# Kernel optimization log

Measured on AMD Instinct MI355X. Metric: run time of the kernel, lower is better.

The kernel has to match this reference:

```python
import jax, jax.numpy as jnp
import numpy as np

N = 100000      # nodes
E = 1250000     # edges
IN = 128        # in_channels
H = 64          # hidden_channels
L = 2           # num_layers (GCNConv count)
EPS = 1e-5      # BatchNorm eps


def setup_inputs() -> dict:
    key = jax.random.key(0)
    ks = jax.random.split(key, 10)
    x = jax.random.normal(ks[0], (N, IN), jnp.float32)
    edge_index = jax.random.randint(ks[1], (2, E), 0, N, dtype=jnp.int32)
    fc_w = jax.random.normal(ks[2], (IN, H), jnp.float32) / np.sqrt(IN)
    fc_b = jax.random.normal(ks[3], (H,), jnp.float32) * 0.01
    conv_w = jax.random.normal(ks[4], (L, H, H), jnp.float32) / np.sqrt(H)
    conv_b = jax.random.normal(ks[5], (L, H), jnp.float32) * 0.01
    bn_gamma = jnp.ones((L + 1, H), jnp.float32)
    bn_beta = jnp.zeros((L + 1, H), jnp.float32)
    bn_mean = jax.random.normal(ks[6], (L + 1, H), jnp.float32) * 0.1
    bn_var = jax.random.uniform(ks[7], (L + 1, H), jnp.float32) + 0.5
    return {"x": x, "edge_index": edge_index, "fc_w": fc_w, "fc_b": fc_b,
            "conv_w": conv_w, "conv_b": conv_b, "bn_gamma": bn_gamma,
            "bn_beta": bn_beta, "bn_mean": bn_mean, "bn_var": bn_var}


def reference(x, edge_index, fc_w, fc_b, conv_w, conv_b, bn_gamma, bn_beta, bn_mean, bn_var):
    n = x.shape[0]
    loops = jnp.arange(n, dtype=edge_index.dtype)
    src = jnp.concatenate([edge_index[0], loops])   # add self-loops (GCNConv default)
    dst = jnp.concatenate([edge_index[1], loops])
    # symmetric normalization: deg computed on destination, norm = d_s^-1/2 * d_d^-1/2
    deg = jax.ops.segment_sum(jnp.ones_like(dst, x.dtype), dst, num_segments=n)
    dis = jax.lax.rsqrt(deg)                        # deg >= 1 thanks to self-loops
    norm = dis[src] * dis[dst]                      # [E+N]

    def bn(h, i):  # eval-mode BatchNorm1d with running stats
        return (h - bn_mean[i]) * (bn_gamma[i] * jax.lax.rsqrt(bn_var[i] + EPS)) + bn_beta[i]

    h = jax.nn.relu(bn(x @ fc_w + fc_b, 0))         # [N, H]; dropout is identity in eval
    last = h
    for i in range(conv_w.shape[0]):
        hw = h @ conv_w[i]                          # GCNConv: transform then aggregate
        agg = jax.ops.segment_sum(hw[src] * norm[:, None], dst, num_segments=n) + conv_b[i]
        h = jax.nn.relu(bn(agg, i + 1)) + last      # residual to post-fc activation
    return h
```

## Files before the change

kernel.cpp:

```cpp
#include <hip/hip_runtime.h>

#define NNODES 100000
#define NEDGES 1250000
#define IN_CH 128
#define HID 64
#define BN_EPS 1e-5f

#define NPAD 100352
#define BIN_N 256
#define BINW 391
#define BIN_CHUNK 2048
#define BIN_BLOCKS 611
#define BIN_CAP_LDS 16
#define BIN_REGION 10000
#define MM_BLOCKS 1563
#define GBLOCKS 3125
#define ELL_C 32
#define OVF_CAP 65536

typedef __attribute__((ext_vector_type(8))) short s16x8;
typedef __attribute__((ext_vector_type(4))) float f32x4;

__device__ __forceinline__ ushort f2bf(float f) {
    union { float f; unsigned int i; } c;
    c.f = f;
    unsigned int lsb = (c.i >> 16) & 1u;
    return (ushort)((c.i + 0x7FFFu + lsb) >> 16);
}
__device__ __forceinline__ float asf(unsigned int i) {
    union { unsigned int i; float f; } c;
    c.i = i;
    return c.f;
}

__device__ __forceinline__ void ell_insert(int d, int soff, int* slot,
                                           int* ell, int* ovf_n, int2* ovf) {
    int s = atomicAdd(&slot[d], 1);
    if (s < ELL_C) ell[(d << 5) + s] = soff;
    else {
        int oi = atomicAdd(ovf_n, 1);
        if (oi < OVF_CAP) ovf[oi] = make_int2(d, soff);
    }
}

__device__ __forceinline__ void fc_body(
        int blk, int tid,
        const float* __restrict__ x, const float* __restrict__ w,
        const float* __restrict__ bb,
        const float* __restrict__ g, const float* __restrict__ be,
        const float* __restrict__ mu, const float* __restrict__ var,
        ushort* __restrict__ h0) {
    const int wave = tid >> 6;
    const int lane = tid & 63;
    const int m = lane & 15;
    const int q = lane >> 4;
    const int node_base = (blk * 4 + wave) * 16;

    s16x8 bfrag[4][4];
#pragma unroll
    for (int kc = 0; kc < 4; ++kc)
#pragma unroll
        for (int ct = 0; ct < 4; ++ct)
#pragma unroll
            for (int j = 0; j < 8; ++j)
                bfrag[kc][ct][j] = (short)f2bf(w[(kc * 32 + q * 8 + j) * HID + ct * 16 + m]);

    f32x4 acc[4] = {{0,0,0,0},{0,0,0,0},{0,0,0,0},{0,0,0,0}};

    int row = node_base + m;
    if (row >= NNODES) row = NNODES - 1;
    const float4* xp = (const float4*)(x + (size_t)row * IN_CH + q * 8);

#pragma unroll
    for (int kc = 0; kc < 4; ++kc) {
        float4 a0 = xp[kc * 8 + 0];
        float4 a1 = xp[kc * 8 + 1];
        s16x8 af;
        af[0] = (short)f2bf(a0.x); af[1] = (short)f2bf(a0.y);
        af[2] = (short)f2bf(a0.z); af[3] = (short)f2bf(a0.w);
        af[4] = (short)f2bf(a1.x); af[5] = (short)f2bf(a1.y);
        af[6] = (short)f2bf(a1.z); af[7] = (short)f2bf(a1.w);
#pragma unroll
        for (int ct = 0; ct < 4; ++ct)
            acc[ct] = __builtin_amdgcn_mfma_f32_16x16x32_bf16(af, bfrag[kc][ct], acc[ct], 0, 0, 0);
    }

#pragma unroll
    for (int ct = 0; ct < 4; ++ct) {
        int col = ct * 16 + m;
        float sc = g[col] * rsqrtf(var[col] + BN_EPS);
        float off = (bb[col] - mu[col]) * sc + be[col];
#pragma unroll
        for (int r = 0; r < 4; ++r) {
            int node = node_base + q * 4 + r;
            if (node < NNODES)
                h0[(size_t)node * HID + col] =
                    f2bf(fmaxf(acc[ct][r] * sc + off, 0.f));
        }
    }
}

__global__ __launch_bounds__(256) void bin_fc(
        const int* __restrict__ src, const int* __restrict__ dst,
        unsigned int* __restrict__ staged, int* bin_n,
        int* slot, int* __restrict__ ell, int* ovf_n, int2* __restrict__ ovf,
        const float* __restrict__ x, const float* __restrict__ w,
        const float* __restrict__ bb,
        const float* __restrict__ g, const float* __restrict__ be,
        const float* __restrict__ mu, const float* __restrict__ var,
        ushort* __restrict__ h0) {
    __shared__ unsigned int sbin[BIN_N][BIN_CAP_LDS];
    __shared__ int scnt[BIN_N];
    __shared__ int sbase[BIN_N];
    const int tid = threadIdx.x;

    if (blockIdx.x >= BIN_BLOCKS) {
        fc_body(blockIdx.x - BIN_BLOCKS, tid, x, w, bb, g, be, mu, var, h0);
        return;
    }

    scnt[tid] = 0;
    __syncthreads();

    const int base = blockIdx.x * (BIN_CHUNK / 4);
    const int4* dst4 = (const int4*)dst;
    const int4* src4 = (const int4*)src;
#pragma unroll
    for (int k = 0; k < BIN_CHUNK / 1024; ++k) {
        int i = base + k * 256 + tid;
        if (i < NEDGES / 4) {
            int4 dv = dst4[i];
            int4 sv = src4[i];
#define BIN_ONE(D, S)                                                       \
            {                                                               \
                int b_ = (D) / BINW;                                        \
                unsigned int pk_ = ((unsigned int)((D) - b_ * BINW) << 17)  \
                                   | (unsigned int)(S);                     \
                int sl_ = atomicAdd(&scnt[b_], 1);                          \
                if (sl_ < BIN_CAP_LDS) sbin[b_][sl_] = pk_;                 \
                else ell_insert((D), (S) << 7, slot, ell, ovf_n, ovf);      \
            }
            BIN_ONE(dv.x, sv.x)
            BIN_ONE(dv.y, sv.y)
            BIN_ONE(dv.z, sv.z)
            BIN_ONE(dv.w, sv.w)
#undef BIN_ONE
        }
    }
    __syncthreads();
    {
        int c = scnt[tid];
        if (c > BIN_CAP_LDS) c = BIN_CAP_LDS;
        sbase[tid] = atomicAdd(&bin_n[tid], c);
    }
    __syncthreads();
    const int wave = tid >> 6;
    const int lane = tid & 63;
    for (int bb2 = wave; bb2 < BIN_N; bb2 += 4) {
        int c = scnt[bb2];
        if (c > BIN_CAP_LDS) c = BIN_CAP_LDS;
        if (lane < c) {
            int gidx = sbase[bb2] + lane;
            unsigned int v = sbin[bb2][lane];
            if (gidx < BIN_REGION) {
                staged[(size_t)bb2 * BIN_REGION + gidx] = v;
            } else {
                int d = bb2 * BINW + (int)(v >> 17);
                ell_insert(d, (int)(v & 0x1FFFFu) << 7, slot, ell, ovf_n, ovf);
            }
        }
    }
}

__global__ __launch_bounds__(256) void ell_fill(
        const unsigned int* __restrict__ staged, const int* __restrict__ bin_n,
        int* slot, int* __restrict__ ell, int* ovf_n, int2* __restrict__ ovf) {
    const int b = blockIdx.x;
    int n = bin_n[b];
    if (n > BIN_REGION) n = BIN_REGION;
    const unsigned int* sp = staged + (size_t)b * BIN_REGION;
    const int lo = b * BINW;
    int i = threadIdx.x;
    for (; i + 768 < n; i += 1024) {
        unsigned int v0 = sp[i];
        unsigned int v1 = sp[i + 256];
        unsigned int v2 = sp[i + 512];
        unsigned int v3 = sp[i + 768];
        ell_insert(lo + (int)(v0 >> 17), (int)(v0 & 0x1FFFFu) << 7, slot, ell, ovf_n, ovf);
        ell_insert(lo + (int)(v1 >> 17), (int)(v1 & 0x1FFFFu) << 7, slot, ell, ovf_n, ovf);
        ell_insert(lo + (int)(v2 >> 17), (int)(v2 & 0x1FFFFu) << 7, slot, ell, ovf_n, ovf);
        ell_insert(lo + (int)(v3 >> 17), (int)(v3 & 0x1FFFFu) << 7, slot, ell, ovf_n, ovf);
    }
    for (; i < n; i += 256) {
        unsigned int v = sp[i];
        ell_insert(lo + (int)(v >> 17), (int)(v & 0x1FFFFu) << 7, slot, ell, ovf_n, ovf);
    }
}

__global__ __launch_bounds__(256) void conv_mm_l1(
        const ushort* __restrict__ h, const float* __restrict__ w,
        const int* __restrict__ deg, ushort* __restrict__ hws) {
    const int tid = threadIdx.x;
    const int wave = tid >> 6;
    const int lane = tid & 63;
    const int m = lane & 15;
    const int q = lane >> 4;
    const int node_base = (blockIdx.x * 4 + wave) * 16;

    s16x8 bfrag[2][4];
#pragma unroll
    for (int kc = 0; kc < 2; ++kc)
#pragma unroll
        for (int ct = 0; ct < 4; ++ct)
#pragma unroll
            for (int j = 0; j < 8; ++j)
                bfrag[kc][ct][j] = (short)f2bf(w[(kc * 32 + q * 8 + j) * HID + ct * 16 + m]);

    f32x4 acc[4] = {{0,0,0,0},{0,0,0,0},{0,0,0,0},{0,0,0,0}};

    int row = node_base + m;
    if (row >= NNODES) row = NNODES - 1;

#pragma unroll
    for (int kc = 0; kc < 2; ++kc) {
        const s16x8* hp = (const s16x8*)(h + (size_t)row * HID + kc * 32 + q * 8);
        s16x8 af = *hp;
#pragma unroll
        for (int ct = 0; ct < 4; ++ct)
            acc[ct] = __builtin_amdgcn_mfma_f32_16x16x32_bf16(af, bfrag[kc][ct], acc[ct], 0, 0, 0);
    }

    float dv[4];
#pragma unroll
    for (int r = 0; r < 4; ++r) {
        int node = node_base + q * 4 + r;
        dv[r] = (node < NNODES) ? rsqrtf((float)(deg[node] + 1)) : 0.f;
    }
#pragma unroll
    for (int ct = 0; ct < 4; ++ct) {
#pragma unroll
        for (int r = 0; r < 4; ++r) {
            int node = node_base + q * 4 + r;
            if (node < NNODES)
                hws[(size_t)node * HID + ct * 16 + m] = f2bf(acc[ct][r] * dv[r]);
        }
    }
}

__global__ __launch_bounds__(256) void conv_mm_l2(
        const ushort* __restrict__ h, const float* __restrict__ w,
        ushort* __restrict__ hws) {
    const int tid = threadIdx.x;
    const int wave = tid >> 6;
    const int lane = tid & 63;
    const int m = lane & 15;
    const int q = lane >> 4;
    const int node_base = (blockIdx.x * 4 + wave) * 16;

    s16x8 bfrag[2][4];
#pragma unroll
    for (int kc = 0; kc < 2; ++kc)
#pragma unroll
        for (int ct = 0; ct < 4; ++ct)
#pragma unroll
            for (int j = 0; j < 8; ++j)
                bfrag[kc][ct][j] = (short)f2bf(w[(kc * 32 + q * 8 + j) * HID + ct * 16 + m]);

    f32x4 acc[4] = {{0,0,0,0},{0,0,0,0},{0,0,0,0},{0,0,0,0}};

    int row = node_base + m;
    if (row >= NNODES) row = NNODES - 1;

#pragma unroll
    for (int kc = 0; kc < 2; ++kc) {
        const s16x8* hp = (const s16x8*)(h + (size_t)row * HID + kc * 32 + q * 8);
        s16x8 af = *hp;
#pragma unroll
        for (int ct = 0; ct < 4; ++ct)
            acc[ct] = __builtin_amdgcn_mfma_f32_16x16x32_bf16(af, bfrag[kc][ct], acc[ct], 0, 0, 0);
    }

#pragma unroll
    for (int ct = 0; ct < 4; ++ct) {
#pragma unroll
        for (int r = 0; r < 4; ++r) {
            int node = node_base + q * 4 + r;
            if (node < NNODES)
                hws[(size_t)node * HID + ct * 16 + m] = f2bf(acc[ct][r]);
        }
    }
}

__global__ __launch_bounds__(256) void gather_update(
        const ushort* __restrict__ hws,
        const int* __restrict__ deg, const int* __restrict__ ell,
        const int* __restrict__ ovf_n, const int2* __restrict__ ovf,
        const float* __restrict__ bias,
        const float* __restrict__ g, const float* __restrict__ be,
        const float* __restrict__ mu, const float* __restrict__ var,
        const ushort* __restrict__ last,
        ushort* __restrict__ out_bf, float* __restrict__ out_f,
        int write_f32) {
    const int wave = threadIdx.x >> 6;
    const int lane = threadIdx.x & 63;
    const int grp  = lane >> 3;
    const int j    = lane & 7;
    const int d = blockIdx.x * 32 + wave * 8 + grp;
    const unsigned int moff = (unsigned int)j * 16u;
    const unsigned int doff = ((unsigned int)d << 7) + moff;

    const char* hb = (const char*)hws;

    float a[8];
    {
        uint4 sv = *(const uint4*)(hb + doff);
        a[0] = asf(sv.x << 16); a[1] = asf(sv.x & 0xffff0000u);
        a[2] = asf(sv.y << 16); a[3] = asf(sv.y & 0xffff0000u);
        a[4] = asf(sv.z << 16); a[5] = asf(sv.z & 0xffff0000u);
        a[6] = asf(sv.w << 16); a[7] = asf(sv.w & 0xffff0000u);
    }

#define ACC8(V)                                                         \
    a[0] += asf((V).x << 16); a[1] += asf((V).x & 0xffff0000u);         \
    a[2] += asf((V).y << 16); a[3] += asf((V).y & 0xffff0000u);         \
    a[4] += asf((V).z << 16); a[5] += asf((V).z & 0xffff0000u);         \
    a[6] += asf((V).w << 16); a[7] += asf((V).w & 0xffff0000u);

    const int n = deg[d];
    const int nn = (n < ELL_C) ? n : ELL_C;
    const int* sp = ell + ((size_t)d << 5);

    int k = 0;
    for (; k + 8 <= nn; k += 8) {
        unsigned int o0 = (unsigned int)sp[k + 0] + moff;
        unsigned int o1 = (unsigned int)sp[k + 1] + moff;
        unsigned int o2 = (unsigned int)sp[k + 2] + moff;
        unsigned int o3 = (unsigned int)sp[k + 3] + moff;
        unsigned int o4 = (unsigned int)sp[k + 4] + moff;
        unsigned int o5 = (unsigned int)sp[k + 5] + moff;
        unsigned int o6 = (unsigned int)sp[k + 6] + moff;
        unsigned int o7 = (unsigned int)sp[k + 7] + moff;
        uint4 v0 = *(const uint4*)(hb + o0);
        uint4 v1 = *(const uint4*)(hb + o1);
        uint4 v2 = *(const uint4*)(hb + o2);
        uint4 v3 = *(const uint4*)(hb + o3);
        uint4 v4 = *(const uint4*)(hb + o4);
        uint4 v5 = *(const uint4*)(hb + o5);
        uint4 v6 = *(const uint4*)(hb + o6);
        uint4 v7 = *(const uint4*)(hb + o7);
        ACC8(v0) ACC8(v1) ACC8(v2) ACC8(v3)
        ACC8(v4) ACC8(v5) ACC8(v6) ACC8(v7)
    }
    for (; k + 4 <= nn; k += 4) {
        unsigned int o0 = (unsigned int)sp[k + 0] + moff;
        unsigned int o1 = (unsigned int)sp[k + 1] + moff;
        unsigned int o2 = (unsigned int)sp[k + 2] + moff;
        unsigned int o3 = (unsigned int)sp[k + 3] + moff;
        uint4 v0 = *(const uint4*)(hb + o0);
        uint4 v1 = *(const uint4*)(hb + o1);
        uint4 v2 = *(const uint4*)(hb + o2);
        uint4 v3 = *(const uint4*)(hb + o3);
        ACC8(v0) ACC8(v1) ACC8(v2) ACC8(v3)
    }
    for (; k < nn; ++k) {
        uint4 v = *(const uint4*)(hb + ((unsigned int)sp[k] + moff));
        ACC8(v)
    }
    if (n > ELL_C) {
        int on = *ovf_n;
        if (on > OVF_CAP) on = OVF_CAP;
        for (int jj = 0; jj < on; ++jj) {
            int2 e = ovf[jj];
            if (e.x == d) {
                uint4 v = *(const uint4*)(hb + ((unsigned int)e.y + moff));
                ACC8(v)
            }
        }
    }
#undef ACC8

    float dd = rsqrtf((float)(n + 1));
    float4 bi0 = ((const float4*)bias)[2 * j], bi1 = ((const float4*)bias)[2 * j + 1];
    float4 g0  = ((const float4*)g)[2 * j],    g1  = ((const float4*)g)[2 * j + 1];
    float4 be0 = ((const float4*)be)[2 * j],   be1 = ((const float4*)be)[2 * j + 1];
    float4 mu0 = ((const float4*)mu)[2 * j],   mu1 = ((const float4*)mu)[2 * j + 1];
    float4 va0 = ((const float4*)var)[2 * j],  va1 = ((const float4*)var)[2 * j + 1];
    uint4 lv = *(const uint4*)((const char*)last + doff);
    float l0 = asf(lv.x << 16), l1 = asf(lv.x & 0xffff0000u);
    float l2 = asf(lv.y << 16), l3 = asf(lv.y & 0xffff0000u);
    float l4 = asf(lv.z << 16), l5 = asf(lv.z & 0xffff0000u);
    float l6 = asf(lv.w << 16), l7 = asf(lv.w & 0xffff0000u);

#define EPI(A, BI, GV, BE, MU, VA, LO) \
    (fmaxf(((A) * dd + (BI) - (MU)) * ((GV) * rsqrtf((VA) + BN_EPS)) + (BE), 0.f) + (LO))
    float r0 = EPI(a[0], bi0.x, g0.x, be0.x, mu0.x, va0.x, l0);
    float r1 = EPI(a[1], bi0.y, g0.y, be0.y, mu0.y, va0.y, l1);
    float r2 = EPI(a[2], bi0.z, g0.z, be0.z, mu0.z, va0.z, l2);
    float r3 = EPI(a[3], bi0.w, g0.w, be0.w, mu0.w, va0.w, l3);
    float r4 = EPI(a[4], bi1.x, g1.x, be1.x, mu1.x, va1.x, l4);
    float r5 = EPI(a[5], bi1.y, g1.y, be1.y, mu1.y, va1.y, l5);
    float r6 = EPI(a[6], bi1.z, g1.z, be1.z, mu1.z, va1.z, l6);
    float r7 = EPI(a[7], bi1.w, g1.w, be1.w, mu1.w, va1.w, l7);
#undef EPI

    if (write_f32) {
        float4* op = (float4*)(out_f + (size_t)d * HID + j * 8);
        op[0] = make_float4(r0, r1, r2, r3);
        op[1] = make_float4(r4, r5, r6, r7);
    } else {
        uint4 o;
        o.x = (unsigned int)f2bf(r0 * dd) | ((unsigned int)f2bf(r1 * dd) << 16);
        o.y = (unsigned int)f2bf(r2 * dd) | ((unsigned int)f2bf(r3 * dd) << 16);
        o.z = (unsigned int)f2bf(r4 * dd) | ((unsigned int)f2bf(r5 * dd) << 16);
        o.w = (unsigned int)f2bf(r6 * dd) | ((unsigned int)f2bf(r7 * dd) << 16);
        *(uint4*)((char*)out_bf + doff) = o;
    }
}

extern "C" void kernel_launch(void* const* d_in, const int* in_sizes, int n_in,
                              void* d_out, int out_size, void* d_ws, size_t ws_size,
                              hipStream_t stream) {
    const float* x      = (const float*)d_in[0];
    const int*   eidx   = (const int*)d_in[1];
    const float* fc_w   = (const float*)d_in[2];
    const float* fc_b   = (const float*)d_in[3];
    const float* conv_w = (const float*)d_in[4];
    const float* conv_b = (const float*)d_in[5];
    const float* bn_g   = (const float*)d_in[6];
    const float* bn_b   = (const float*)d_in[7];
    const float* bn_m   = (const float*)d_in[8];
    const float* bn_v   = (const float*)d_in[9];

    const int* src = eidx;
    const int* dst = eidx + NEDGES;
    float* out = (float*)d_out;

    int*    slot    = (int*)d_ws;
    int*    meta    = slot + NPAD;
    int*    ovf_n   = meta;
    int*    bin_n   = meta + 16;
    int2*   ovf     = (int2*)(meta + 272);
    int*    ell     = (int*)(ovf + OVF_CAP);
    ushort* h0      = (ushort*)(ell + (size_t)NNODES * ELL_C);
    ushort* h1      = h0 + (size_t)NNODES * HID;
    ushort* hws     = h1 + (size_t)NNODES * HID;
    unsigned int* staged = (unsigned int*)(hws + (size_t)NNODES * HID);

    const int BLK = 256;

    hipMemsetAsync(slot, 0, (size_t)(NPAD + 272) * 4, stream);

    bin_fc<<<BIN_BLOCKS + MM_BLOCKS, BLK, 0, stream>>>(
        src, dst, staged, bin_n, slot, ell, ovf_n, ovf,
        x, fc_w, fc_b, bn_g, bn_b, bn_m, bn_v, h0);

    ell_fill<<<BIN_N, BLK, 0, stream>>>(staged, bin_n, slot, ell, ovf_n, ovf);

    conv_mm_l1<<<MM_BLOCKS, BLK, 0, stream>>>(h0, conv_w, slot, hws);

    gather_update<<<GBLOCKS, BLK, 0, stream>>>(hws, slot, ell, ovf_n, ovf,
                                               conv_b, bn_g + HID, bn_b + HID,
                                               bn_m + HID, bn_v + HID, h0,
                                               h1, nullptr, 0);

    conv_mm_l2<<<MM_BLOCKS, BLK, 0, stream>>>(h1, conv_w + HID * HID, hws);

    gather_update<<<GBLOCKS, BLK, 0, stream>>>(hws, slot, ell, ovf_n, ovf,
                                               conv_b + HID, bn_g + 2 * HID, bn_b + 2 * HID,
                                               bn_m + 2 * HID, bn_v + 2 * HID,
                                               h0, nullptr, out, 1);
}
```

Measured before the change: 276.4 us.

## Fuse layer-2 dense transform into layer-1 gather epilogue via LDS tile

The first gather/update kernel now stages its 32 bf16 output rows in shared memory and immediately runs the layer-2 64x64 MFMA transform on them, writing the transformed features directly. This removes the separate conv_mm_l2 launch and the global round trip of the intermediate h1 activations. In exchange, each gather block adds a syncthreads, LDS usage and per-block reloading and conversion of the weight fragments, which could reduce occupancy of the latency-bound gather.

New measurement: 271.4 us. About the same (-1.8%).

```diff
diff --git a/kernel.cpp b/kernel.cpp
--- a/kernel.cpp
+++ b/kernel.cpp
@@ -247,51 +247,7 @@
     }
 }
 
-__global__ __launch_bounds__(256) void conv_mm_l2(
-        const ushort* __restrict__ h, const float* __restrict__ w,
-        ushort* __restrict__ hws) {
-    const int tid = threadIdx.x;
-    const int wave = tid >> 6;
-    const int lane = tid & 63;
-    const int m = lane & 15;
-    const int q = lane >> 4;
-    const int node_base = (blockIdx.x * 4 + wave) * 16;
-
-    s16x8 bfrag[2][4];
-#pragma unroll
-    for (int kc = 0; kc < 2; ++kc)
-#pragma unroll
-        for (int ct = 0; ct < 4; ++ct)
-#pragma unroll
-            for (int j = 0; j < 8; ++j)
-                bfrag[kc][ct][j] = (short)f2bf(w[(kc * 32 + q * 8 + j) * HID + ct * 16 + m]);
-
-    f32x4 acc[4] = {{0,0,0,0},{0,0,0,0},{0,0,0,0},{0,0,0,0}};
-
-    int row = node_base + m;
-    if (row >= NNODES) row = NNODES - 1;
-
-#pragma unroll
-    for (int kc = 0; kc < 2; ++kc) {
-        const s16x8* hp = (const s16x8*)(h + (size_t)row * HID + kc * 32 + q * 8);
-        s16x8 af = *hp;
-#pragma unroll
-        for (int ct = 0; ct < 4; ++ct)
-            acc[ct] = __builtin_amdgcn_mfma_f32_16x16x32_bf16(af, bfrag[kc][ct], acc[ct], 0, 0, 0);
-    }
-
-#pragma unroll
-    for (int ct = 0; ct < 4; ++ct) {
-#pragma unroll
-        for (int r = 0; r < 4; ++r) {
-            int node = node_base + q * 4 + r;
-            if (node < NNODES)
-                hws[(size_t)node * HID + ct * 16 + m] = f2bf(acc[ct][r]);
-        }
-    }
-}
-
-__global__ __launch_bounds__(256) void gather_update(
+__global__ __launch_bounds__(256) void gather_conv(
         const ushort* __restrict__ hws,
         const int* __restrict__ deg, const int* __restrict__ ell,
         const int* __restrict__ ovf_n, const int2* __restrict__ ovf,
@@ -299,8 +255,9 @@
         const float* __restrict__ g, const float* __restrict__ be,
         const float* __restrict__ mu, const float* __restrict__ var,
         const ushort* __restrict__ last,
-        ushort* __restrict__ out_bf, float* __restrict__ out_f,
-        int write_f32) {
+        const float* __restrict__ w2,
+        ushort* __restrict__ hws2) {
+    __shared__ ushort sh[32][72];
     const int wave = threadIdx.x >> 6;
     const int lane = threadIdx.x & 63;
     const int grp  = lane >> 3;
@@ -403,18 +360,170 @@
     float r7 = EPI(a[7], bi1.w, g1.w, be1.w, mu1.w, va1.w, l7);
 #undef EPI
 
-    if (write_f32) {
-        float4* op = (float4*)(out_f + (size_t)d * HID + j * 8);
-        op[0] = make_float4(r0, r1, r2, r3);
-        op[1] = make_float4(r4, r5, r6, r7);
-    } else {
+    {
+        const int rloc = wave * 8 + grp;
         uint4 o;
         o.x = (unsigned int)f2bf(r0 * dd) | ((unsigned int)f2bf(r1 * dd) << 16);
         o.y = (unsigned int)f2bf(r2 * dd) | ((unsigned int)f2bf(r3 * dd) << 16);
         o.z = (unsigned int)f2bf(r4 * dd) | ((unsigned int)f2bf(r5 * dd) << 16);
         o.w = (unsigned int)f2bf(r6 * dd) | ((unsigned int)f2bf(r7 * dd) << 16);
-        *(uint4*)((char*)out_bf + doff) = o;
-    }
+        *(uint4*)(&sh[rloc][j * 8]) = o;
+    }
+    __syncthreads();
+
+    {
+        const int rt = wave >> 1;
+        const int cbase = (wave & 1) * 2;
+        const int m = lane & 15;
+        const int q = lane >> 4;
+
+        s16x8 bfrag[2][2];
+#pragma unroll
+        for (int kc = 0; kc < 2; ++kc)
+#pragma unroll
+            for (int c = 0; c < 2; ++c)
+#pragma unroll
+                for (int jj = 0; jj < 8; ++jj)
+                    bfrag[kc][c][jj] = (short)f2bf(
+                        w2[(kc * 32 + q * 8 + jj) * HID + (cbase + c) * 16 + m]);
+
+        f32x4 acc2[2] = {{0,0,0,0},{0,0,0,0}};
+#pragma unroll
+        for (int kc = 0; kc < 2; ++kc) {
+            s16x8 af = *(const s16x8*)(&sh[rt * 16 + m][kc * 32 + q * 8]);
+#pragma unroll
+            for (int c = 0; c < 2; ++c)
+                acc2[c] = __builtin_amdgcn_mfma_f32_16x16x32_bf16(
+                    af, bfrag[kc][c], acc2[c], 0, 0, 0);
+        }
+
+        const int node_base = blockIdx.x * 32 + rt * 16;
+#pragma unroll
+        for (int c = 0; c < 2; ++c) {
+            const int col = (cbase + c) * 16 + m;
+#pragma unroll
+            for (int r = 0; r < 4; ++r) {
+                int node = node_base + q * 4 + r;
+                hws2[(size_t)node * HID + col] = f2bf(acc2[c][r]);
+            }
+        }
+    }
+}
+
+__global__ __launch_bounds__(256) void gather_update(
+        const ushort* __restrict__ hws,
+        const int* __restrict__ deg, const int* __restrict__ ell,
+        const int* __restrict__ ovf_n, const int2* __restrict__ ovf,
+        const float* __restrict__ bias,
+        const float* __restrict__ g, const float* __restrict__ be,
+        const float* __restrict__ mu, const float* __restrict__ var,
+        const ushort* __restrict__ last,
+        float* __restrict__ out_f) {
+    const int wave = threadIdx.x >> 6;
+    const int lane = threadIdx.x & 63;
+    const int grp  = lane >> 3;
+    const int j    = lane & 7;
+    const int d = blockIdx.x * 32 + wave * 8 + grp;
+    const unsigned int moff = (unsigned int)j * 16u;
+    const unsigned int doff = ((unsigned int)d << 7) + moff;
+
+    const char* hb = (const char*)hws;
+
+    float a[8];
+    {
+        uint4 sv = *(const uint4*)(hb + doff);
+        a[0] = asf(sv.x << 16); a[1] = asf(sv.x & 0xffff0000u);
+        a[2] = asf(sv.y << 16); a[3] = asf(sv.y & 0xffff0000u);
+        a[4] = asf(sv.z << 16); a[5] = asf(sv.z & 0xffff0000u);
+        a[6] = asf(sv.w << 16); a[7] = asf(sv.w & 0xffff0000u);
+    }
+
+#define ACC8(V)                                                         \
+    a[0] += asf((V).x << 16); a[1] += asf((V).x & 0xffff0000u);         \
+    a[2] += asf((V).y << 16); a[3] += asf((V).y & 0xffff0000u);         \
+    a[4] += asf((V).z << 16); a[5] += asf((V).z & 0xffff0000u);         \
+    a[6] += asf((V).w << 16); a[7] += asf((V).w & 0xffff0000u);
+
+    const int n = deg[d];
+    const int nn = (n < ELL_C) ? n : ELL_C;
+    const int* sp = ell + ((size_t)d << 5);
+
+    int k = 0;
+    for (; k + 8 <= nn; k += 8) {
+        unsigned int o0 = (unsigned int)sp[k + 0] + moff;
+        unsigned int o1 = (unsigned int)sp[k + 1] + moff;
+        unsigned int o2 = (unsigned int)sp[k + 2] + moff;
+        unsigned int o3 = (unsigned int)sp[k + 3] + moff;
+        unsigned int o4 = (unsigned int)sp[k + 4] + moff;
+        unsigned int o5 = (unsigned int)sp[k + 5] + moff;
+        unsigned int o6 = (unsigned int)sp[k + 6] + moff;
+        unsigned int o7 = (unsigned int)sp[k + 7] + moff;
+        uint4 v0 = *(const uint4*)(hb + o0);
+        uint4 v1 = *(const uint4*)(hb + o1);
+        uint4 v2 = *(const uint4*)(hb + o2);
+        uint4 v3 = *(const uint4*)(hb + o3);
+        uint4 v4 = *(const uint4*)(hb + o4);
+        uint4 v5 = *(const uint4*)(hb + o5);
+        uint4 v6 = *(const uint4*)(hb + o6);
+        uint4 v7 = *(const uint4*)(hb + o7);
+        ACC8(v0) ACC8(v1) ACC8(v2) ACC8(v3)
+        ACC8(v4) ACC8(v5) ACC8(v6) ACC8(v7)
+    }
+    for (; k + 4 <= nn; k += 4) {
+        unsigned int o0 = (unsigned int)sp[k + 0] + moff;
+        unsigned int o1 = (unsigned int)sp[k + 1] + moff;
+        unsigned int o2 = (unsigned int)sp[k + 2] + moff;
+        unsigned int o3 = (unsigned int)sp[k + 3] + moff;
+        uint4 v0 = *(const uint4*)(hb + o0);
+        uint4 v1 = *(const uint4*)(hb + o1);
+        uint4 v2 = *(const uint4*)(hb + o2);
+        uint4 v3 = *(const uint4*)(hb + o3);
+        ACC8(v0) ACC8(v1) ACC8(v2) ACC8(v3)
+    }
+    for (; k < nn; ++k) {
+        uint4 v = *(const uint4*)(hb + ((unsigned int)sp[k] + moff));
+        ACC8(v)
+    }
+    if (n > ELL_C) {
+        int on = *ovf_n;
+        if (on > OVF_CAP) on = OVF_CAP;
+        for (int jj = 0; jj < on; ++jj) {
+            int2 e = ovf[jj];
+            if (e.x == d) {
+                uint4 v = *(const uint4*)(hb + ((unsigned int)e.y + moff));
+                ACC8(v)
+            }
+        }
+    }
+#undef ACC8
+
+    float dd = rsqrtf((float)(n + 1));
+    float4 bi0 = ((const float4*)bias)[2 * j], bi1 = ((const float4*)bias)[2 * j + 1];
+    float4 g0  = ((const float4*)g)[2 * j],    g1  = ((const float4*)g)[2 * j + 1];
+    float4 be0 = ((const float4*)be)[2 * j],   be1 = ((const float4*)be)[2 * j + 1];
+    float4 mu0 = ((const float4*)mu)[2 * j],   mu1 = ((const float4*)mu)[2 * j + 1];
+    float4 va0 = ((const float4*)var)[2 * j],  va1 = ((const float4*)var)[2 * j + 1];
+    uint4 lv = *(const uint4*)((const char*)last + doff);
+    float l0 = asf(lv.x << 16), l1 = asf(lv.x & 0xffff0000u);
+    float l2 = asf(lv.y << 16), l3 = asf(lv.y & 0xffff0000u);
+    float l4 = asf(lv.z << 16), l5 = asf(lv.z & 0xffff0000u);
+    float l6 = asf(lv.w << 16), l7 = asf(lv.w & 0xffff0000u);
+
+#define EPI(A, BI, GV, BE, MU, VA, LO) \
+    (fmaxf(((A) * dd + (BI) - (MU)) * ((GV) * rsqrtf((VA) + BN_EPS)) + (BE), 0.f) + (LO))
+    float r0 = EPI(a[0], bi0.x, g0.x, be0.x, mu0.x, va0.x, l0);
+    float r1 = EPI(a[1], bi0.y, g0.y, be0.y, mu0.y, va0.y, l1);
+    float r2 = EPI(a[2], bi0.z, g0.z, be0.z, mu0.z, va0.z, l2);
+    float r3 = EPI(a[3], bi0.w, g0.w, be0.w, mu0.w, va0.w, l3);
+    float r4 = EPI(a[4], bi1.x, g1.x, be1.x, mu1.x, va1.x, l4);
+    float r5 = EPI(a[5], bi1.y, g1.y, be1.y, mu1.y, va1.y, l5);
+    float r6 = EPI(a[6], bi1.z, g1.z, be1.z, mu1.z, va1.z, l6);
+    float r7 = EPI(a[7], bi1.w, g1.w, be1.w, mu1.w, va1.w, l7);
+#undef EPI
+
+    float4* op = (float4*)(out_f + (size_t)d * HID + j * 8);
+    op[0] = make_float4(r0, r1, r2, r3);
+    op[1] = make_float4(r4, r5, r6, r7);
 }
 
 extern "C" void kernel_launch(void* const* d_in, const int* in_sizes, int n_in,
@@ -442,8 +551,8 @@
     int2*   ovf     = (int2*)(meta + 272);
     int*    ell     = (int*)(ovf + OVF_CAP);
     ushort* h0      = (ushort*)(ell + (size_t)NNODES * ELL_C);
-    ushort* h1      = h0 + (size_t)NNODES * HID;
-    ushort* hws     = h1 + (size_t)NNODES * HID;
+    ushort* hws2    = h0 + (size_t)NNODES * HID;
+    ushort* hws     = hws2 + (size_t)NNODES * HID;
     unsigned int* staged = (unsigned int*)(hws + (size_t)NNODES * HID);
 
     const int BLK = 256;
@@ -458,15 +567,13 @@
 
     conv_mm_l1<<<MM_BLOCKS, BLK, 0, stream>>>(h0, conv_w, slot, hws);
 
-    gather_update<<<GBLOCKS, BLK, 0, stream>>>(hws, slot, ell, ovf_n, ovf,
-                                               conv_b, bn_g + HID, bn_b + HID,
-                                               bn_m + HID, bn_v + HID, h0,
-                                               h1, nullptr, 0);
-
-    conv_mm_l2<<<MM_BLOCKS, BLK, 0, stream>>>(h1, conv_w + HID * HID, hws);
-
-    gather_update<<<GBLOCKS, BLK, 0, stream>>>(hws, slot, ell, ovf_n, ovf,
+    gather_conv<<<GBLOCKS, BLK, 0, stream>>>(hws, slot, ell, ovf_n, ovf,
+                                             conv_b, bn_g + HID, bn_b + HID,
+                                             bn_m + HID, bn_v + HID, h0,
+                                             conv_w + HID * HID, hws2);
+
+    gather_update<<<GBLOCKS, BLK, 0, stream>>>(hws2, slot, ell, ovf_n, ovf,
                                                conv_b + HID, bn_g + 2 * HID, bn_b + 2 * HID,
                                                bn_m + 2 * HID, bn_v + 2 * HID,
-                                               h0, nullptr, out, 1);
-}
+                                               h0, out);
+}
```
